# Kernel optimization log

Hardware: AMD Instinct MI355X
Metric: run time of the kernel (lower is better)

Reference implementation:

```python
import jax, jax.numpy as jnp
import numpy as np

B, N1, N2 = 16, 256, 256
FA, FE = 128, 128  # n_atom_feature, n_edge_feature


def setup_inputs() -> dict:
    key = jax.random.key(0)
    ks = jax.random.split(key, 8)
    x1 = jax.random.normal(ks[0], (B, N1, FA), dtype=jnp.float32)
    x2 = jax.random.normal(ks[1], (B, N2, FA), dtype=jnp.float32)
    edge = jax.random.normal(ks[2], (B, N1, N2, FE), dtype=jnp.float32)
    valid_edge = jax.random.randint(ks[3], (B, N1, N2), 0, 2).astype(jnp.float32)
    s_w = 1.0 / np.sqrt(FA)
    s_m = 1.0 / np.sqrt(FE + FA)
    W_w = jax.random.uniform(ks[4], (FA, FA), jnp.float32, -s_w, s_w)      # [in, out]
    W_b = jax.random.uniform(ks[5], (FA,), jnp.float32, -s_w, s_w)
    M_w = jax.random.uniform(ks[6], (FE + FA, FA), jnp.float32, -s_m, s_m)  # [in, out]
    M_b = jax.random.uniform(ks[7], (FA,), jnp.float32, -s_m, s_m)
    return {"x1": x1, "x2": x2, "edge": edge, "valid_edge": valid_edge,
            "W_w": W_w, "W_b": W_b, "M_w": M_w, "M_b": M_b}


def reference(x1, x2, edge, valid_edge, W_w, W_b, M_w, M_b):
    # m1 = W(x1): [B, N1, FA]
    m1 = jnp.einsum('bif,fg->big', x1, W_w) + W_b
    # M(new_edge) without materializing concat: split M into x2-part and edge-part.
    # new_edge = cat([broadcast(x2) -> [B,N1,N2,FA], edge], -1)
    Mw_x2 = M_w[:FA]    # [FA, FA]
    Mw_e = M_w[FA:]     # [FE, FA]
    me = jnp.einsum('bije,eg->bijg', edge, Mw_e)                 # [B,N1,N2,FA]
    mx2 = jnp.einsum('bjf,fg->bjg', x2, Mw_x2)                   # [B,N2,FA]
    m_edge = me + mx2[:, None, :, :] + M_b                       # [B,N1,N2,FA]
    # mask-multiply then max over neighbor axis (axis=2), as in the original
    m2 = jnp.max(m_edge * valid_edge[..., None], axis=2)         # [B,N1,FA]
    return jax.nn.relu(m1 + m2)
```

## Files before the change

kernel.cpp:

```cpp
#include <hip/hip_runtime.h>
#include <hip/hip_bf16.h>

#define BB 16
#define N1 256
#define N2 256
#define FA 128
#define FE 128

typedef __attribute__((ext_vector_type(8))) short bf16x8;
typedef __attribute__((ext_vector_type(4))) float f32x4;

static __device__ __forceinline__ unsigned short f2bf(float f) {
    union { float f; unsigned int u; } v; v.f = f;
    unsigned int u = v.u;
    unsigned int r = (u + 0x7FFFu + ((u >> 16) & 1u)) >> 16;
    return (unsigned short)r;
}

static __device__ __forceinline__ bf16x8 pack8(float4 lo, float4 hi) {
    bf16x8 r;
    r[0] = (short)f2bf(lo.x); r[1] = (short)f2bf(lo.y);
    r[2] = (short)f2bf(lo.z); r[3] = (short)f2bf(lo.w);
    r[4] = (short)f2bf(hi.x); r[5] = (short)f2bf(hi.y);
    r[6] = (short)f2bf(hi.z); r[7] = (short)f2bf(hi.w);
    return r;
}

__global__ __launch_bounds__(128) void prep_gemm(const float* __restrict__ x,
                                                 const float* __restrict__ W,
                                                 const float* __restrict__ bias,
                                                 float* __restrict__ out) {
    __shared__ float xs[8][128];
    const int r0 = blockIdx.x * 8;
    const int g = threadIdx.x;
    #pragma unroll
    for (int r = 0; r < 8; ++r)
        xs[r][g] = x[(size_t)(r0 + r) * FA + g];
    __syncthreads();
    float acc[8];
    const float bv = bias[g];
    #pragma unroll
    for (int r = 0; r < 8; ++r) acc[r] = bv;
    #pragma unroll 8
    for (int f = 0; f < 128; ++f) {
        const float wv = W[f * FA + g];
        #pragma unroll
        for (int r = 0; r < 8; ++r) acc[r] += xs[r][f] * wv;
    }
    #pragma unroll
    for (int r = 0; r < 8; ++r)
        out[(size_t)(r0 + r) * FA + g] = acc[r];
}

__global__ __launch_bounds__(128) void prep_gemm_T(const float* __restrict__ x,
                                                   const float* __restrict__ W,
                                                   const float* __restrict__ bias,
                                                   float* __restrict__ outT) {
    __shared__ float xs[8][128];
    const int r0 = blockIdx.x * 8;
    const int b = r0 >> 8;
    const int j0 = r0 & 255;
    const int g = threadIdx.x;
    #pragma unroll
    for (int r = 0; r < 8; ++r)
        xs[r][g] = x[(size_t)(r0 + r) * FA + g];
    __syncthreads();
    float acc[8];
    const float bv = bias[g];
    #pragma unroll
    for (int r = 0; r < 8; ++r) acc[r] = bv;
    #pragma unroll 8
    for (int f = 0; f < 128; ++f) {
        const float wv = W[f * FA + g];
        #pragma unroll
        for (int r = 0; r < 8; ++r) acc[r] += xs[r][f] * wv;
    }
    float4 v0 = {acc[0], acc[1], acc[2], acc[3]};
    float4 v1 = {acc[4], acc[5], acc[6], acc[7]};
    float4* dst = (float4*)&outT[(size_t)(b * 128 + g) * 256 + j0];
    dst[0] = v0;
    dst[1] = v1;
}

__global__ __launch_bounds__(256) void prep_wt(const float* __restrict__ Mw,
                                               unsigned short* __restrict__ wT) {
    const int idx = blockIdx.x * 256 + threadIdx.x;
    const int g = idx >> 7, e = idx & 127;
    wT[idx] = f2bf(Mw[(size_t)(FA + e) * FA + g]);
}

__global__ __launch_bounds__(256, 2) void edge_main(
    const float* __restrict__ edge,
    const float* __restrict__ valid,
    const float* __restrict__ mx2bT,
    const unsigned short* __restrict__ wT,
    float* __restrict__ out)
{
    const int tid = threadIdx.x;
    const int wv = tid >> 6;
    const int lane = tid & 63;
    const int n = lane & 15, q = lane >> 4;
    const int bi = blockIdx.x * 4 + wv;
    const int b = bi >> 8;

    bf16x8 bF[8][4];
    #pragma unroll
    for (int t = 0; t < 8; ++t)
        #pragma unroll
        for (int s = 0; s < 4; ++s)
            bF[t][s] = *(const bf16x8*)&wT[(t * 16 + n) * FE + s * 32 + q * 8];

    float runmax[8];
    #pragma unroll
    for (int t = 0; t < 8; ++t) runmax[t] = -3.0e38f;

    const float* eb  = edge + (size_t)bi * (N2 * FE);
    const float* mxT = mx2bT + (size_t)b * (N2 * FA);
    const float* vb  = valid + (size_t)bi * N2;

    for (int strip = 0; strip < 16; ++strip) {
        const int j0 = strip * 16;

        const float* erow = eb + (size_t)(j0 + n) * FE + q * 8;
        float4 a[8];
        #pragma unroll
        for (int s = 0; s < 4; ++s) {
            a[2 * s]     = *(const float4*)(erow + s * 32);
            a[2 * s + 1] = *(const float4*)(erow + s * 32 + 4);
        }
        const float4 vld = *(const float4*)(vb + j0 + q * 4);
        float4 mxv[8];
        #pragma unroll
        for (int t = 0; t < 8; ++t)
            mxv[t] = *(const float4*)(mxT + (size_t)(t * 16 + n) * N2 + j0 + q * 4);

        bf16x8 aF[4];
        #pragma unroll
        for (int s = 0; s < 4; ++s)
            aF[s] = pack8(a[2 * s], a[2 * s + 1]);

        #pragma unroll
        for (int t = 0; t < 8; ++t) {
            f32x4 acc = {0.f, 0.f, 0.f, 0.f};
            #pragma unroll
            for (int s = 0; s < 4; ++s)
                acc = __builtin_amdgcn_mfma_f32_16x16x32_bf16(aF[s], bF[t][s], acc, 0, 0, 0);
            float v0 = (acc[0] + mxv[t].x) * vld.x;
            float v1 = (acc[1] + mxv[t].y) * vld.y;
            float v2 = (acc[2] + mxv[t].z) * vld.z;
            float v3 = (acc[3] + mxv[t].w) * vld.w;
            runmax[t] = fmaxf(runmax[t], fmaxf(fmaxf(v0, v1), fmaxf(v2, v3)));
        }
    }

    #pragma unroll
    for (int t = 0; t < 8; ++t) {
        float m = runmax[t];
        m = fmaxf(m, __shfl_xor(m, 16, 64));
        m = fmaxf(m, __shfl_xor(m, 32, 64));
        runmax[t] = m;
    }
    if (lane < 16) {
        #pragma unroll
        for (int t = 0; t < 8; ++t) {
            const size_t o = (size_t)bi * FA + t * 16 + lane;
            const float m1 = out[o];
            out[o] = fmaxf(m1 + runmax[t], 0.0f);
        }
    }
}

extern "C" void kernel_launch(void* const* d_in, const int* in_sizes, int n_in,
                              void* d_out, int out_size, void* d_ws, size_t ws_size,
                              hipStream_t stream) {
    const float* x1    = (const float*)d_in[0];
    const float* x2    = (const float*)d_in[1];
    const float* edge  = (const float*)d_in[2];
    const float* valid = (const float*)d_in[3];
    const float* W_w   = (const float*)d_in[4];
    const float* W_b   = (const float*)d_in[5];
    const float* M_w   = (const float*)d_in[6];
    const float* M_b   = (const float*)d_in[7];
    float* out = (float*)d_out;

    unsigned short* wT = (unsigned short*)d_ws;
    float* mx2bT = (float*)((char*)d_ws + 32768);

    prep_gemm<<<BB * N1 / 8, 128, 0, stream>>>(x1, W_w, W_b, out);
    prep_gemm_T<<<BB * N2 / 8, 128, 0, stream>>>(x2, M_w, M_b, mx2bT);
    prep_wt<<<64, 256, 0, stream>>>(M_w, wT);
    edge_main<<<BB * N1 / 4, 256, 0, stream>>>(edge, valid, mx2bT, wT, out);
}
```

Measured before the change: 743.6 us.

## Split output features across waves and stage edge tiles in shared memory

Each block now handles a single (b,i) row instead of four, and its four waves split the 128 output features two tiles apiece. Edge strips are loaded cooperatively, converted to bf16 and double-buffered in swizzled LDS so all waves share one load. This cuts per-wave register pressure (8 to 2 B-fragment tiles), which is why the occupancy hint rises to 3. The cost is a block barrier every strip and four times as many blocks. The kernel is memory-bound on the 537MB edge tensor, so the gain depends mostly on better latency hiding.

```diff
diff --git a/kernel.cpp b/kernel.cpp
--- a/kernel.cpp
+++ b/kernel.cpp
@@ -89,83 +89,106 @@
     wT[idx] = f2bf(Mw[(size_t)(FA + e) * FA + g]);
 }
 
-__global__ __launch_bounds__(256, 2) void edge_main(
+__global__ __launch_bounds__(256, 3) void edge_main(
     const float* __restrict__ edge,
     const float* __restrict__ valid,
     const float* __restrict__ mx2bT,
     const unsigned short* __restrict__ wT,
     float* __restrict__ out)
 {
+    __shared__ __align__(16) unsigned short ebuf[2][2048];
+
     const int tid = threadIdx.x;
     const int wv = tid >> 6;
     const int lane = tid & 63;
     const int n = lane & 15, q = lane >> 4;
-    const int bi = blockIdx.x * 4 + wv;
+    const int bi = blockIdx.x;
     const int b = bi >> 8;
 
-    bf16x8 bF[8][4];
-    #pragma unroll
-    for (int t = 0; t < 8; ++t)
+    bf16x8 bF[2][4];
+    #pragma unroll
+    for (int tt = 0; tt < 2; ++tt) {
+        const int t = wv * 2 + tt;
         #pragma unroll
         for (int s = 0; s < 4; ++s)
-            bF[t][s] = *(const bf16x8*)&wT[(t * 16 + n) * FE + s * 32 + q * 8];
-
-    float runmax[8];
-    #pragma unroll
-    for (int t = 0; t < 8; ++t) runmax[t] = -3.0e38f;
+            bF[tt][s] = *(const bf16x8*)&wT[(t * 16 + n) * FE + s * 32 + q * 8];
+    }
 
     const float* eb  = edge + (size_t)bi * (N2 * FE);
     const float* mxT = mx2bT + (size_t)b * (N2 * FA);
     const float* vb  = valid + (size_t)bi * N2;
 
+    const int sj = tid >> 4;
+    const int se = (tid & 15) * 8;
+    const float* sg = eb + (size_t)sj * FE + se;
+    char* ebase = (char*)&ebuf[0][0];
+    const int sphys = (tid * 16) ^ ((sj & 7) << 4);
+
+    {
+        float4 v0 = *(const float4*)(sg);
+        float4 v1 = *(const float4*)(sg + 4);
+        *(bf16x8*)(ebase + sphys) = pack8(v0, v1);
+    }
+    __syncthreads();
+
+    float runmax[2] = {-3.0e38f, -3.0e38f};
+
+    const int lq = n * 256 + q * 16;
+    const int xsw = (n & 7) << 4;
+
     for (int strip = 0; strip < 16; ++strip) {
         const int j0 = strip * 16;
-
-        const float* erow = eb + (size_t)(j0 + n) * FE + q * 8;
-        float4 a[8];
-        #pragma unroll
-        for (int s = 0; s < 4; ++s) {
-            a[2 * s]     = *(const float4*)(erow + s * 32);
-            a[2 * s + 1] = *(const float4*)(erow + s * 32 + 4);
-        }
+        const bool more = (strip + 1) < 16;
+
+        float4 p0, p1;
+        if (more) {
+            const float* nsg = sg + (size_t)(j0 + 16) * FE;
+            p0 = *(const float4*)(nsg);
+            p1 = *(const float4*)(nsg + 4);
+        }
+
         const float4 vld = *(const float4*)(vb + j0 + q * 4);
-        float4 mxv[8];
-        #pragma unroll
-        for (int t = 0; t < 8; ++t)
-            mxv[t] = *(const float4*)(mxT + (size_t)(t * 16 + n) * N2 + j0 + q * 4);
-
+        float4 mxv[2];
+        #pragma unroll
+        for (int tt = 0; tt < 2; ++tt) {
+            const int t = wv * 2 + tt;
+            mxv[tt] = *(const float4*)(mxT + (size_t)(t * 16 + n) * N2 + j0 + q * 4);
+        }
+
+        char* cbuf = ebase + (strip & 1) * 4096;
         bf16x8 aF[4];
         #pragma unroll
         for (int s = 0; s < 4; ++s)
-            aF[s] = pack8(a[2 * s], a[2 * s + 1]);
-
-        #pragma unroll
-        for (int t = 0; t < 8; ++t) {
+            aF[s] = *(const bf16x8*)(cbuf + ((lq + s * 64) ^ xsw));
+
+        #pragma unroll
+        for (int tt = 0; tt < 2; ++tt) {
             f32x4 acc = {0.f, 0.f, 0.f, 0.f};
             #pragma unroll
             for (int s = 0; s < 4; ++s)
-                acc = __builtin_amdgcn_mfma_f32_16x16x32_bf16(aF[s], bF[t][s], acc, 0, 0, 0);
-            float v0 = (acc[0] + mxv[t].x) * vld.x;
-            float v1 = (acc[1] + mxv[t].y) * vld.y;
-            float v2 = (acc[2] + mxv[t].z) * vld.z;
-            float v3 = (acc[3] + mxv[t].w) * vld.w;
-            runmax[t] = fmaxf(runmax[t], fmaxf(fmaxf(v0, v1), fmaxf(v2, v3)));
-        }
-    }
-
-    #pragma unroll
-    for (int t = 0; t < 8; ++t) {
-        float m = runmax[t];
+                acc = __builtin_amdgcn_mfma_f32_16x16x32_bf16(aF[s], bF[tt][s], acc, 0, 0, 0);
+            float v0 = (acc[0] + mxv[tt].x) * vld.x;
+            float v1 = (acc[1] + mxv[tt].y) * vld.y;
+            float v2 = (acc[2] + mxv[tt].z) * vld.z;
+            float v3 = (acc[3] + mxv[tt].w) * vld.w;
+            runmax[tt] = fmaxf(runmax[tt], fmaxf(fmaxf(v0, v1), fmaxf(v2, v3)));
+        }
+
+        if (more) {
+            *(bf16x8*)(ebase + (((strip + 1) & 1) * 4096) + sphys) = pack8(p0, p1);
+        }
+        __syncthreads();
+    }
+
+    #pragma unroll
+    for (int tt = 0; tt < 2; ++tt) {
+        float m = runmax[tt];
         m = fmaxf(m, __shfl_xor(m, 16, 64));
         m = fmaxf(m, __shfl_xor(m, 32, 64));
-        runmax[t] = m;
-    }
-    if (lane < 16) {
-        #pragma unroll
-        for (int t = 0; t < 8; ++t) {
+        if (lane < 16) {
+            const int t = wv * 2 + tt;
             const size_t o = (size_t)bi * FA + t * 16 + lane;
-            const float m1 = out[o];
-            out[o] = fmaxf(m1 + runmax[t], 0.0f);
+            out[o] = fmaxf(out[o] + m, 0.0f);
         }
     }
 }
@@ -189,5 +212,5 @@
     prep_gemm<<<BB * N1 / 8, 128, 0, stream>>>(x1, W_w, W_b, out);
     prep_gemm_T<<<BB * N2 / 8, 128, 0, stream>>>(x2, M_w, M_b, mx2bT);
     prep_wt<<<64, 256, 0, stream>>>(M_w, wT);
-    edge_main<<<BB * N1 / 4, 256, 0, stream>>>(edge, valid, mx2bT, wT, out);
-}
+    edge_main<<<BB * N1, 256, 0, stream>>>(edge, valid, mx2bT, wT, out);
+}
```

After: 753.7 us. No clear change (+1.4%).
